# Kernel tuning notes

Hardware: AMD Instinct MI355X
Metric: run time of the kernel (lower is better)

The kernel has to match this reference:

```python
import jax, jax.numpy as jnp
import numpy as np

MV_DIM = 8
# basis index -> blade bitmask (e1=1,e2=2,e3=4): [1, e1, e2, e3, e12, e13, e23, e123]
_ORDER = [0, 1, 2, 4, 3, 5, 6, 7]

def _cayley():
    idx_of = {m: i for i, m in enumerate(_ORDER)}
    C = np.zeros((8, 8, 8), np.float32)
    for i, a in enumerate(_ORDER):
        for j, b in enumerate(_ORDER):
            s, n = 0, a >> 1
            while n:
                s += bin(n & b).count('1')
                n >>= 1
            C[i, j, idx_of[a ^ b]] = -1.0 if (s & 1) else 1.0
    return jnp.asarray(C)

C_GP = _cayley()
# reverse signs per grade [0,1,1,1,2,2,2,3] -> (-1)^(g(g-1)/2)
REV = jnp.asarray([1., 1., 1., 1., -1., -1., -1., -1.], jnp.float32)

def rotor_sandwich(R, mv):
    # R: [G,8], mv: [N,G,8] -> R * mv * ~R per group
    Rrev = R * REV
    t = jnp.einsum('gi,ngj,ijk->ngk', R, mv, C_GP)
    return jnp.einsum('ngi,gj,ijk->ngk', t, Rrev, C_GP)


def setup_inputs() -> dict:
    key = jax.random.key(0)
    k1, k2, k3 = jax.random.split(key, 3)
    N, d, G, K = 8192, 768, 256, 16
    x = jax.random.normal(k1, (N, d), jnp.float32)
    # Lloyd-Max style 1-D codebook over [-1,1] (unit-vector components)
    centroids = jnp.linspace(-1.0, 1.0, K, dtype=jnp.float32)
    # random rotors: cos(t/2) + sin(t/2)*B, B unit bivector (indices 4,5,6)
    theta = jax.random.uniform(k2, (G,), jnp.float32, 0.0, np.pi)
    bv = jax.random.normal(k3, (G, 3), jnp.float32)
    bv = bv / jnp.linalg.norm(bv, axis=-1, keepdims=True)
    rotors = jnp.zeros((G, MV_DIM), jnp.float32)
    rotors = rotors.at[:, 0].set(jnp.cos(theta / 2))
    rotors = rotors.at[:, 4:7].set(jnp.sin(theta / 2)[:, None] * bv)
    return {"x": x, "centroids": centroids, "rotors": rotors}


def reference(x, centroids, rotors):
    N, d = x.shape
    G = rotors.shape[0]
    # quantize
    norms = jnp.clip(jnp.linalg.norm(x, axis=-1, keepdims=True), 1e-8)  # [N,1]
    x_unit = x / norms
    mv = jnp.zeros((N, G, MV_DIM), x.dtype).at[..., 1:4].set(x_unit.reshape(N, G, 3))
    mv_rot = rotor_sandwich(rotors, mv)
    flat = mv_rot[..., 1:4].reshape(N, G * 3)                 # [N,d]
    idx = jnp.argmin(jnp.abs(flat[..., None] - centroids), axis=-1)  # [N,d]
    # dequantize from indices
    vals = centroids[idx].reshape(N, G, 3)
    mv_q = jnp.zeros((N, G, MV_DIM), x.dtype).at[..., 1:4].set(vals)
    mv_recon = rotor_sandwich(rotors * REV, mv_q)             # unapply
    x_hat = mv_recon[..., 1:4].reshape(N, d)[:, :d] * norms
    return x_hat, idx, norms[:, 0]
```

## Files before the change

### kernel.cpp

```cpp
#include <hip/hip_runtime.h>


__device__ __constant__ int c_ORD[8] = {0, 1, 2, 4, 3, 5, 6, 7};

__device__ __forceinline__ double csign(int a, int b) {
    int s = 0, n = a >> 1;
    while (n) { s += __popc(n & b); n >>= 1; }
    return (s & 1) ? -1.0 : 1.0;
}

__global__ void build_rotor_mats(const float* __restrict__ rotors,
                                 double* __restrict__ matsD,
                                 float* __restrict__ matsF, int G) {
    int t = blockIdx.x * blockDim.x + threadIdx.x;
    if (t >= G * 6) return;
    const int g = t / 6;
    const int rem = t % 6;
    const int pass = rem / 3;
    const int m = rem % 3 + 1;
    const double REV[8] = {1, 1, 1, 1, -1, -1, -1, -1};
    double R[8], Rr[8];
    for (int i = 0; i < 8; i++) {
        R[i]  = (double)rotors[g * 8 + i];
        Rr[i] = R[i] * REV[i];
    }
    const double* L = pass ? Rr : R;
    const double* Q = pass ? R  : Rr;
    const int am = c_ORD[m];
    double tv[8];
    for (int i = 0; i < 8; i++) tv[i] = 0.0;
    for (int p = 0; p < 8; p++) {
        int ap = c_ORD[p];
        tv[c_ORD[ap ^ am]] += L[p] * csign(ap, am);
    }
    double wc[8];
    for (int i = 0; i < 8; i++) wc[i] = 0.0;
    for (int i = 0; i < 8; i++) {
        int ai = c_ORD[i];
        for (int j = 0; j < 8; j++) {
            int aj = c_ORD[j];
            wc[c_ORD[ai ^ aj]] += tv[i] * Q[j] * csign(ai, aj);
        }
    }
    for (int k = 1; k <= 3; k++) {
        if (pass == 0)
            matsD[(size_t)g * 9 + (k - 1) * 3 + (m - 1)] = wc[k];
        else
            matsF[(size_t)g * 9 + (k - 1) * 3 + (m - 1)] = (float)wc[k];
    }
}

__global__ __launch_bounds__(256, 4) void rotor_quant(
    const float* __restrict__ x, const float* __restrict__ cents,
    const double* __restrict__ matsD, const float* __restrict__ matsF,
    float* __restrict__ out_xhat, float* __restrict__ out_idx,
    float* __restrict__ out_norm, int N, int G, int K) {
    const int tid = threadIdx.x;
    const int lane = tid & 63;
    const int wid = tid >> 6;
    const int n = blockIdx.x * 4 + wid;
    const int d = 3 * G;

    __shared__ float csf[16];
    __shared__ double mid[15];
    if (tid < K) csf[tid] = cents[tid];
    if (tid < K - 1)
        mid[tid] = 0.5 * ((double)cents[tid] + (double)cents[tid + 1]);
    __syncthreads();
    if (n >= N) return;

    const float4* xrow = (const float4*)(x + (size_t)n * d) + lane * 3;
    float4 xa = xrow[0], xb = xrow[1], xc = xrow[2];
    float xf[12] = {xa.x, xa.y, xa.z, xa.w, xb.x, xb.y, xb.z, xb.w,
                    xc.x, xc.y, xc.z, xc.w};

    double ss = 0.0;
#pragma unroll
    for (int i = 0; i < 12; i++) {
        double v = (double)xf[i];
        ss += v * v;
    }
#pragma unroll
    for (int off = 32; off > 0; off >>= 1) ss += __shfl_xor(ss, off, 64);
    double nn = sqrt(ss);
    if (nn < 1e-8) nn = 1e-8;
    const double inv = 1.0 / nn;
    const float normf = (float)nn;

    const double scale = 0.5 * (double)(K - 1);
    float oh[12], oq[12];
#pragma unroll
    for (int j = 0; j < 4; j++) {
        const int g = 4 * lane + j;
        const double* M = matsD + (size_t)g * 9;
        const double x0 = (double)xf[3 * j], x1 = (double)xf[3 * j + 1],
                     x2 = (double)xf[3 * j + 2];
        double w[3];
#pragma unroll
        for (int k = 0; k < 3; k++)
            w[k] = (M[3 * k] * x0 + M[3 * k + 1] * x1 + M[3 * k + 2] * x2) * inv;

        int qi[3];
        float v[3];
#pragma unroll
        for (int c = 0; c < 3; c++) {
            int i = (int)((w[c] + 1.0) * scale + 0.5);
            i = min(K - 1, max(0, i));
            if (i > 0 && w[c] <= mid[i - 1]) i -= 1;
            else if (i < K - 1 && w[c] > mid[i]) i += 1;
            qi[c] = i;
            v[c] = csf[i];
        }

        const float* Mr = matsF + (size_t)g * 9;
        oh[3 * j]     = (Mr[0] * v[0] + Mr[1] * v[1] + Mr[2] * v[2]) * normf;
        oh[3 * j + 1] = (Mr[3] * v[0] + Mr[4] * v[1] + Mr[5] * v[2]) * normf;
        oh[3 * j + 2] = (Mr[6] * v[0] + Mr[7] * v[1] + Mr[8] * v[2]) * normf;
        oq[3 * j]     = (float)qi[0];
        oq[3 * j + 1] = (float)qi[1];
        oq[3 * j + 2] = (float)qi[2];
    }

    float4* oxh = (float4*)(out_xhat + (size_t)n * d) + lane * 3;
    float4* oix = (float4*)(out_idx + (size_t)n * d) + lane * 3;
    oxh[0] = make_float4(oh[0], oh[1], oh[2], oh[3]);
    oxh[1] = make_float4(oh[4], oh[5], oh[6], oh[7]);
    oxh[2] = make_float4(oh[8], oh[9], oh[10], oh[11]);
    oix[0] = make_float4(oq[0], oq[1], oq[2], oq[3]);
    oix[1] = make_float4(oq[4], oq[5], oq[6], oq[7]);
    oix[2] = make_float4(oq[8], oq[9], oq[10], oq[11]);
    if (lane == 0) out_norm[n] = normf;
}

extern "C" void kernel_launch(void* const* d_in, const int* in_sizes, int n_in,
                              void* d_out, int out_size, void* d_ws, size_t ws_size,
                              hipStream_t stream) {
    const float* x      = (const float*)d_in[0];
    const float* cents  = (const float*)d_in[1];
    const float* rotors = (const float*)d_in[2];
    const int K = in_sizes[1];
    const int G = in_sizes[2] / 8;
    const int d = 3 * G;
    const int N = in_sizes[0] / d;

    double* matsD = (double*)d_ws;
    float*  matsF = (float*)(matsD + (size_t)G * 9);

    build_rotor_mats<<<(G * 6 + 255) / 256, 256, 0, stream>>>(rotors, matsD,
                                                              matsF, G);

    float* out = (float*)d_out;
    float* out_xhat = out;
    float* out_idx  = out + (size_t)N * d;
    float* out_norm = out + (size_t)2 * N * d;
    rotor_quant<<<(N + 3) / 4, 256, 0, stream>>>(x, cents, matsD, matsF,
                                                 out_xhat, out_idx, out_norm,
                                                 N, G, K);
}
```

Baseline: 113.8 us.

## Fuse rotor matrix construction into quant kernel via closed-form rotation

Drops the separate build_rotor_mats launch. Each thread now computes the 3x3 rotation matrix directly from the rotor's scalar and bivector components using a closed-form quaternion-style formula. The inverse sandwich is applied as the transpose of that matrix. This removes a kernel launch and the gathered reads of per-group double and float matrices from workspace, at the cost of extra FP64 arithmetic recomputed in every thread. It also assumes rotors hold only grade-0 and grade-2 parts, which matches how the inputs are built.

After: 99.11 us. 12.9% less time.

```diff
diff --git a/kernel.cpp b/kernel.cpp
--- a/kernel.cpp
+++ b/kernel.cpp
@@ -1,58 +1,9 @@
 #include <hip/hip_runtime.h>
 
 
-__device__ __constant__ int c_ORD[8] = {0, 1, 2, 4, 3, 5, 6, 7};
-
-__device__ __forceinline__ double csign(int a, int b) {
-    int s = 0, n = a >> 1;
-    while (n) { s += __popc(n & b); n >>= 1; }
-    return (s & 1) ? -1.0 : 1.0;
-}
-
-__global__ void build_rotor_mats(const float* __restrict__ rotors,
-                                 double* __restrict__ matsD,
-                                 float* __restrict__ matsF, int G) {
-    int t = blockIdx.x * blockDim.x + threadIdx.x;
-    if (t >= G * 6) return;
-    const int g = t / 6;
-    const int rem = t % 6;
-    const int pass = rem / 3;
-    const int m = rem % 3 + 1;
-    const double REV[8] = {1, 1, 1, 1, -1, -1, -1, -1};
-    double R[8], Rr[8];
-    for (int i = 0; i < 8; i++) {
-        R[i]  = (double)rotors[g * 8 + i];
-        Rr[i] = R[i] * REV[i];
-    }
-    const double* L = pass ? Rr : R;
-    const double* Q = pass ? R  : Rr;
-    const int am = c_ORD[m];
-    double tv[8];
-    for (int i = 0; i < 8; i++) tv[i] = 0.0;
-    for (int p = 0; p < 8; p++) {
-        int ap = c_ORD[p];
-        tv[c_ORD[ap ^ am]] += L[p] * csign(ap, am);
-    }
-    double wc[8];
-    for (int i = 0; i < 8; i++) wc[i] = 0.0;
-    for (int i = 0; i < 8; i++) {
-        int ai = c_ORD[i];
-        for (int j = 0; j < 8; j++) {
-            int aj = c_ORD[j];
-            wc[c_ORD[ai ^ aj]] += tv[i] * Q[j] * csign(ai, aj);
-        }
-    }
-    for (int k = 1; k <= 3; k++) {
-        if (pass == 0)
-            matsD[(size_t)g * 9 + (k - 1) * 3 + (m - 1)] = wc[k];
-        else
-            matsF[(size_t)g * 9 + (k - 1) * 3 + (m - 1)] = (float)wc[k];
-    }
-}
-
 __global__ __launch_bounds__(256, 4) void rotor_quant(
     const float* __restrict__ x, const float* __restrict__ cents,
-    const double* __restrict__ matsD, const float* __restrict__ matsF,
+    const float* __restrict__ rotors,
     float* __restrict__ out_xhat, float* __restrict__ out_idx,
     float* __restrict__ out_norm, int N, int G, int K) {
     const int tid = threadIdx.x;
@@ -88,17 +39,34 @@
     const float normf = (float)nn;
 
     const double scale = 0.5 * (double)(K - 1);
+    const float4* rot4 = (const float4*)rotors;
     float oh[12], oq[12];
 #pragma unroll
     for (int j = 0; j < 4; j++) {
         const int g = 4 * lane + j;
-        const double* M = matsD + (size_t)g * 9;
+        float4 r0 = rot4[2 * g];
+        float4 r1 = rot4[2 * g + 1];
+        const double A = (double)r0.x, P = (double)r1.x,
+                     Q = (double)r1.y, R = (double)r1.z;
+        const double aa = A * A, pp = P * P, qq = Q * Q, rr = R * R;
+        const double ap = A * P, aq = A * Q, ar = A * R;
+        const double pq = P * Q, pr = P * R, qr = Q * R;
+        const double m00 = aa - pp - qq + rr;
+        const double m01 = 2.0 * (ap - qr);
+        const double m02 = 2.0 * (aq + pr);
+        const double m10 = -2.0 * (ap + qr);
+        const double m11 = aa - pp + qq - rr;
+        const double m12 = 2.0 * (ar - pq);
+        const double m20 = 2.0 * (pr - aq);
+        const double m21 = -2.0 * (ar + pq);
+        const double m22 = aa + pp - qq - rr;
+
         const double x0 = (double)xf[3 * j], x1 = (double)xf[3 * j + 1],
                      x2 = (double)xf[3 * j + 2];
         double w[3];
-#pragma unroll
-        for (int k = 0; k < 3; k++)
-            w[k] = (M[3 * k] * x0 + M[3 * k + 1] * x1 + M[3 * k + 2] * x2) * inv;
+        w[0] = (m00 * x0 + m01 * x1 + m02 * x2) * inv;
+        w[1] = (m10 * x0 + m11 * x1 + m12 * x2) * inv;
+        w[2] = (m20 * x0 + m21 * x1 + m22 * x2) * inv;
 
         int qi[3];
         float v[3];
@@ -112,10 +80,12 @@
             v[c] = csf[i];
         }
 
-        const float* Mr = matsF + (size_t)g * 9;
-        oh[3 * j]     = (Mr[0] * v[0] + Mr[1] * v[1] + Mr[2] * v[2]) * normf;
-        oh[3 * j + 1] = (Mr[3] * v[0] + Mr[4] * v[1] + Mr[5] * v[2]) * normf;
-        oh[3 * j + 2] = (Mr[6] * v[0] + Mr[7] * v[1] + Mr[8] * v[2]) * normf;
+        const float f00 = (float)m00, f01 = (float)m01, f02 = (float)m02;
+        const float f10 = (float)m10, f11 = (float)m11, f12 = (float)m12;
+        const float f20 = (float)m20, f21 = (float)m21, f22 = (float)m22;
+        oh[3 * j]     = (f00 * v[0] + f10 * v[1] + f20 * v[2]) * normf;
+        oh[3 * j + 1] = (f01 * v[0] + f11 * v[1] + f21 * v[2]) * normf;
+        oh[3 * j + 2] = (f02 * v[0] + f12 * v[1] + f22 * v[2]) * normf;
         oq[3 * j]     = (float)qi[0];
         oq[3 * j + 1] = (float)qi[1];
         oq[3 * j + 2] = (float)qi[2];
@@ -143,17 +113,10 @@
     const int d = 3 * G;
     const int N = in_sizes[0] / d;
 
-    double* matsD = (double*)d_ws;
-    float*  matsF = (float*)(matsD + (size_t)G * 9);
-
-    build_rotor_mats<<<(G * 6 + 255) / 256, 256, 0, stream>>>(rotors, matsD,
-                                                              matsF, G);
-
     float* out = (float*)d_out;
     float* out_xhat = out;
     float* out_idx  = out + (size_t)N * d;
     float* out_norm = out + (size_t)2 * N * d;
-    rotor_quant<<<(N + 3) / 4, 256, 0, stream>>>(x, cents, matsD, matsF,
-                                                 out_xhat, out_idx, out_norm,
-                                                 N, G, K);
+    rotor_quant<<<(N + 3) / 4, 256, 0, stream>>>(x, cents, rotors, out_xhat,
+                                                 out_idx, out_norm, N, G, K);
 }
```
